# Kernel optimization log

Measured on AMD Instinct MI355X. Metric: run time of the kernel, lower is better.

Reference implementation:

```python
import jax, jax.numpy as jnp
import numpy as np

B, S, D, U = 64, 2048, 512, 512

def setup_inputs() -> dict:
    key = jax.random.key(0)
    ks = jax.random.split(key, 8)
    query = jax.random.normal(ks[0], (B, D), dtype=jnp.float32)
    values = jax.random.normal(ks[1], (B, S, D), dtype=jnp.float32)
    # Keras Dense params (glorot-like scale), with biases (Dense default use_bias=True)
    W1 = jax.random.normal(ks[2], (D, U), dtype=jnp.float32) / np.sqrt(D)
    b1 = jnp.zeros((U,), dtype=jnp.float32)
    W2 = jax.random.normal(ks[3], (D, U), dtype=jnp.float32) / np.sqrt(D)
    b2 = jnp.zeros((U,), dtype=jnp.float32)
    V = jax.random.normal(ks[4], (U, 1), dtype=jnp.float32) / np.sqrt(U)
    bv = jnp.zeros((1,), dtype=jnp.float32)
    return {"query": query, "values": values, "W1": W1, "b1": b1,
            "W2": W2, "b2": b2, "V": V, "bv": bv}

def reference(query, values, W1, b1, W2, b2, V, bv) -> jnp.ndarray:
    # query: [B, D], values: [B, S, D]
    q_proj = query @ W1 + b1                      # [B, U]
    v_proj = jnp.einsum('bsd,du->bsu', values, W2) + b2  # [B, S, U]
    h = jnp.tanh(q_proj[:, None, :] + v_proj)     # [B, S, U]
    scores = jnp.einsum('bsu,uo->bso', h, V) + bv # [B, S, 1]
    attn = jax.nn.softmax(scores, axis=1)         # softmax over sequence axis
    context = jnp.sum(attn * values, axis=1)      # [B, D]
    return context
```

## Files before the change

kernel.cpp:

```cpp
#include <hip/hip_runtime.h>
#include <hip/hip_bf16.h>

#define BB 64
#define SS 2048
#define DD 512
#define UU 512
#define BS (BB*SS)

typedef __attribute__((ext_vector_type(8))) short bf16x8;
typedef __attribute__((ext_vector_type(4))) float f32x4;

static __device__ __forceinline__ unsigned short f2bf(float x) {
    union { float f; unsigned int u; } v; v.f = x;
    unsigned int r = v.u + 0x7FFFu + ((v.u >> 16) & 1u);
    return (unsigned short)(r >> 16);
}

__global__ void k_prep(const float* __restrict__ W2, unsigned short* __restrict__ W2T,
                       const float* __restrict__ query, const float* __restrict__ W1,
                       const float* __restrict__ b1, const float* __restrict__ b2,
                       float* __restrict__ qpb) {
    __shared__ float tile[64][65];
    const int t = threadIdx.x;
    if (blockIdx.x < 64) {
        const int ti = blockIdx.x >> 3;
        const int tj = blockIdx.x & 7;
        #pragma unroll
        for (int i = 0; i < 16; ++i) {
            int e = i*256 + t;
            int dr = e >> 6, uc = e & 63;
            tile[dr][uc] = W2[(size_t)(ti*64+dr)*UU + tj*64+uc];
        }
        __syncthreads();
        #pragma unroll
        for (int i = 0; i < 16; ++i) {
            int e = i*256 + t;
            int ur = e >> 6, dc = e & 63;
            W2T[(size_t)(tj*64+ur)*DD + ti*64+dc] = f2bf(tile[dc][ur]);
        }
    } else {
        const int b = blockIdx.x - 64;
        float a0 = 0.f, a1 = 0.f;
        for (int d = 0; d < DD; ++d) {
            float q = query[b*DD + d];
            a0 += q * W1[(size_t)d*UU + t];
            a1 += q * W1[(size_t)d*UU + t + 256];
        }
        qpb[b*UU + t]       = a0 + b1[t]     + b2[t];
        qpb[b*UU + t + 256] = a1 + b1[t+256] + b2[t+256];
    }
}

__launch_bounds__(256, 2)
__global__ void k_scores(const float* __restrict__ values,
                         const unsigned short* __restrict__ W2T,
                         const float* __restrict__ qpb,
                         const float* __restrict__ Vw,
                         float* __restrict__ scores) {
    __shared__ unsigned short Albuf[64*512];
    const int t  = threadIdx.x;
    const int m0 = blockIdx.x * 64;
    const int b  = m0 >> 11;

    const int wave = t >> 6, lane = t & 63;
    const int ln15 = lane & 15, quad = lane >> 4;

    float qv[2][4], vw[2][4];
    #pragma unroll
    for (int nc = 0; nc < 2; ++nc)
        #pragma unroll
        for (int nt = 0; nt < 4; ++nt) {
            int n = nc*256 + wave*64 + nt*16 + ln15;
            qv[nc][nt] = qpb[b*UU + n];
            vw[nc][nt] = Vw[n];
        }

    const float* src = values + (size_t)m0 * DD;
    #pragma unroll
    for (int i = 0; i < 16; ++i) {
        int gf  = i*256 + t;
        int row = gf >> 6;
        int g   = gf & 63;
        const float4 f0 = *(const float4*)(src + (size_t)row*DD + g*8);
        const float4 f1 = *(const float4*)(src + (size_t)row*DD + g*8 + 4);
        ushort4 lo, hi;
        lo.x = f2bf(f0.x); lo.y = f2bf(f0.y); lo.z = f2bf(f0.z); lo.w = f2bf(f0.w);
        hi.x = f2bf(f1.x); hi.y = f2bf(f1.y); hi.z = f2bf(f1.z); hi.w = f2bf(f1.w);
        int gs = g ^ (row & 7);
        ushort4* dst = (ushort4*)&Albuf[row*512 + gs*8];
        dst[0] = lo; dst[1] = hi;
    }
    __syncthreads();

    const unsigned short* bp[4];
    #pragma unroll
    for (int nt = 0; nt < 4; ++nt)
        bp[nt] = W2T + (size_t)(wave*64 + nt*16 + ln15) * DD + quad*8;

    int abase[4];
    #pragma unroll
    for (int mt = 0; mt < 4; ++mt)
        abase[mt] = (mt*16 + ln15) * 512;
    const int xm = ln15 & 7;

    float sacc[4][4] = {};

    bf16x8 bb[2][4];
    #pragma unroll
    for (int nt = 0; nt < 4; ++nt)
        bb[0][nt] = *(const bf16x8*)(bp[nt]);

    for (int nc = 0; nc < 2; ++nc) {
        f32x4 acc[4][4];
        #pragma unroll
        for (int mt = 0; mt < 4; ++mt)
            #pragma unroll
            for (int nt = 0; nt < 4; ++nt)
                acc[mt][nt] = f32x4{0.f, 0.f, 0.f, 0.f};

        #pragma unroll
        for (int ks = 0; ks < 16; ++ks) {
            const int j   = nc*16 + ks;
            const int cur = j & 1;
            if (j + 1 < 32) {
                const int jn  = j + 1;
                const int off = (jn >> 4) * (256*DD) + (jn & 15) * 32;
                #pragma unroll
                for (int nt = 0; nt < 4; ++nt)
                    bb[cur ^ 1][nt] = *(const bf16x8*)(bp[nt] + off);
            }
            bf16x8 afr[4];
            const int g4 = ks*4 + quad;
            #pragma unroll
            for (int mt = 0; mt < 4; ++mt)
                afr[mt] = *(const bf16x8*)&Albuf[abase[mt] + ((g4 ^ xm) << 3)];
            #pragma unroll
            for (int mt = 0; mt < 4; ++mt)
                #pragma unroll
                for (int nt = 0; nt < 4; ++nt)
                    acc[mt][nt] = __builtin_amdgcn_mfma_f32_16x16x32_bf16(
                        afr[mt], bb[cur][nt], acc[mt][nt], 0, 0, 0);
        }

        #pragma unroll
        for (int nt = 0; nt < 4; ++nt) {
            const float q = qv[nc][nt];
            const float w = vw[nc][nt];
            #pragma unroll
            for (int mt = 0; mt < 4; ++mt)
                #pragma unroll
                for (int r = 0; r < 4; ++r) {
                    float x = q + acc[mt][nt][r];
                    float e = __expf(x + x);
                    float rc = __builtin_amdgcn_rcpf(e + 1.f);
                    sacc[mt][r] = fmaf(fmaf(-2.f, rc, 1.f), w, sacc[mt][r]);
                }
        }
    }

    __syncthreads();
    float* buf = (float*)Albuf;
    #pragma unroll
    for (int mt = 0; mt < 4; ++mt)
        #pragma unroll
        for (int r = 0; r < 4; ++r) {
            float v = sacc[mt][r];
            v += __shfl_xor(v, 1);
            v += __shfl_xor(v, 2);
            v += __shfl_xor(v, 4);
            v += __shfl_xor(v, 8);
            if (ln15 == 0) buf[wave*64 + mt*16 + quad*4 + r] = v;
        }
    __syncthreads();
    if (t < 64)
        scores[m0 + t] = buf[t] + buf[64 + t] + buf[128 + t] + buf[192 + t];
}

__launch_bounds__(256)
__global__ void k_context(const float* __restrict__ values, const float* __restrict__ scores,
                          float* __restrict__ out) {
    __shared__ float w[SS];
    __shared__ float red8[8];
    __shared__ float4 red[16][16];
    const int blk = blockIdx.x;
    const int b = blk >> 3, d0 = (blk & 7) * 64;
    const int t = threadIdx.x;

    const float* sc = scores + b*SS;
    float v[8];
    float mx = -1e30f;
    #pragma unroll
    for (int i = 0; i < 8; ++i) { v[i] = sc[i*256 + t]; mx = fmaxf(mx, v[i]); }
    #pragma unroll
    for (int off = 32; off; off >>= 1) mx = fmaxf(mx, __shfl_xor(mx, off));
    if ((t & 63) == 0) red8[t >> 6] = mx;
    __syncthreads();
    mx = fmaxf(fmaxf(red8[0], red8[1]), fmaxf(red8[2], red8[3]));
    float sum = 0.f;
    #pragma unroll
    for (int i = 0; i < 8; ++i) { v[i] = __expf(v[i] - mx); sum += v[i]; }
    #pragma unroll
    for (int off = 32; off; off >>= 1) sum += __shfl_xor(sum, off);
    __syncthreads();
    if ((t & 63) == 0) red8[4 + (t >> 6)] = sum;
    __syncthreads();
    sum = red8[4] + red8[5] + red8[6] + red8[7];
    float inv = 1.f / sum;
    #pragma unroll
    for (int i = 0; i < 8; ++i) w[i*256 + t] = v[i] * inv;
    __syncthreads();

    const int di = t & 15, sg = t >> 4;
    float4 acc = make_float4(0.f, 0.f, 0.f, 0.f);
    const float* vb = values + (size_t)b*SS*DD + d0 + di*4;
    #pragma unroll 8
    for (int s = sg; s < SS; s += 16) {
        float wgt = w[s];
        float4 vv = *(const float4*)(vb + (size_t)s*DD);
        acc.x += wgt*vv.x; acc.y += wgt*vv.y; acc.z += wgt*vv.z; acc.w += wgt*vv.w;
    }
    red[sg][di] = acc;
    __syncthreads();
    if (t < 16) {
        float4 s4 = make_float4(0.f, 0.f, 0.f, 0.f);
        #pragma unroll
        for (int g = 0; g < 16; ++g) {
            float4 vv = red[g][t];
            s4.x += vv.x; s4.y += vv.y; s4.z += vv.z; s4.w += vv.w;
        }
        *(float4*)(out + (size_t)b*DD + d0 + t*4) = s4;
    }
}

extern "C" void kernel_launch(void* const* d_in, const int* in_sizes, int n_in,
                              void* d_out, int out_size, void* d_ws, size_t ws_size,
                              hipStream_t stream) {
    const float* query  = (const float*)d_in[0];
    const float* values = (const float*)d_in[1];
    const float* W1     = (const float*)d_in[2];
    const float* b1     = (const float*)d_in[3];
    const float* W2     = (const float*)d_in[4];
    const float* b2     = (const float*)d_in[5];
    const float* Vw     = (const float*)d_in[6];

    char* ws = (char*)d_ws;
    unsigned short* W2T = (unsigned short*)ws;
    float* qpb    = (float*)(ws + 524288);
    float* scores = (float*)(ws + 524288 + 131072);
    float* out    = (float*)d_out;

    k_prep<<<128, 256, 0, stream>>>(W2, W2T, query, W1, b1, b2, qpb);
    k_scores<<<BS/64, 256, 0, stream>>>(values, W2T, qpb, Vw, scores);
    k_context<<<BB*8, 256, 0, stream>>>(values, scores, out);
}
```

Measured before the change: 585.0 us.

## Fuse context accumulation into scores kernel with split softmax and 32x32 MFMA

The scores kernel now computes a block-local softmax (max, sum) over its 64 rows and immediately accumulates the weighted sum of the values rows it already has cached, writing partial context vectors. A small finish kernel then combines the 32 partials per batch with a log-sum-exp rescale. This removes the second full pass over the values tensor from global memory. The GEMM also switches to 32x32x16 MFMA with W2 pre-swizzled into a fragment-ordered layout, so B fragments are loaded with contiguous per-lane reads. The cost is extra partial-buffer traffic and a slightly different order of floating-point summation.

```diff
diff --git a/kernel.cpp b/kernel.cpp
--- a/kernel.cpp
+++ b/kernel.cpp
@@ -8,7 +8,7 @@
 #define BS (BB*SS)
 
 typedef __attribute__((ext_vector_type(8))) short bf16x8;
-typedef __attribute__((ext_vector_type(4))) float f32x4;
+typedef __attribute__((ext_vector_type(16))) float f32x16;
 
 static __device__ __forceinline__ unsigned short f2bf(float x) {
     union { float f; unsigned int u; } v; v.f = x;
@@ -16,7 +16,7 @@
     return (unsigned short)(r >> 16);
 }
 
-__global__ void k_prep(const float* __restrict__ W2, unsigned short* __restrict__ W2T,
+__global__ void k_prep(const float* __restrict__ W2, unsigned short* __restrict__ W2F,
                        const float* __restrict__ query, const float* __restrict__ W1,
                        const float* __restrict__ b1, const float* __restrict__ b2,
                        float* __restrict__ qpb) {
@@ -32,11 +32,17 @@
             tile[dr][uc] = W2[(size_t)(ti*64+dr)*UU + tj*64+uc];
         }
         __syncthreads();
-        #pragma unroll
-        for (int i = 0; i < 16; ++i) {
-            int e = i*256 + t;
-            int ur = e >> 6, dc = e & 63;
-            W2T[(size_t)(tj*64+ur)*DD + ti*64+dc] = f2bf(tile[dc][ur]);
+        const int ksl = t >> 6, ln = t & 63;
+        const int lh = ln >> 5, l31 = ln & 31;
+        #pragma unroll
+        for (int ntl = 0; ntl < 2; ++ntl) {
+            const int ks = ti*4 + ksl;
+            const int ntile = tj*2 + ntl;
+            bf16x8 g;
+            #pragma unroll
+            for (int j = 0; j < 8; ++j)
+                g[j] = (short)f2bf(tile[ksl*16 + lh*8 + j][ntl*32 + l31]);
+            *(bf16x8*)&W2F[(size_t)(((ks*16 + ntile)*64 + ln) * 8)] = g;
         }
     } else {
         const int b = blockIdx.x - 64;
@@ -53,27 +59,35 @@
 
 __launch_bounds__(256, 2)
 __global__ void k_scores(const float* __restrict__ values,
-                         const unsigned short* __restrict__ W2T,
+                         const unsigned short* __restrict__ W2F,
                          const float* __restrict__ qpb,
                          const float* __restrict__ Vw,
-                         float* __restrict__ scores) {
+                         float* __restrict__ pm, float* __restrict__ pl,
+                         float* __restrict__ pv) {
     __shared__ unsigned short Albuf[64*512];
-    const int t  = threadIdx.x;
-    const int m0 = blockIdx.x * 64;
-    const int b  = m0 >> 11;
-
+    const int t   = threadIdx.x;
+    const int blk = blockIdx.x;
+    const int m0  = blk * 64;
+    const int b   = blk >> 5;
     const int wave = t >> 6, lane = t & 63;
-    const int ln15 = lane & 15, quad = lane >> 4;
-
-    float qv[2][4], vw[2][4];
-    #pragma unroll
-    for (int nc = 0; nc < 2; ++nc)
-        #pragma unroll
-        for (int nt = 0; nt < 4; ++nt) {
-            int n = nc*256 + wave*64 + nt*16 + ln15;
-            qv[nc][nt] = qpb[b*UU + n];
-            vw[nc][nt] = Vw[n];
-        }
+    const int ln31 = lane & 31, half = lane >> 5;
+
+    const bf16x8* Bp = (const bf16x8*)W2F;
+    bf16x8 bfr[2][4];
+    #pragma unroll
+    for (int nt = 0; nt < 4; ++nt)
+        bfr[0][nt] = Bp[(0*16 + wave*4 + nt)*64 + lane];
+    #pragma unroll
+    for (int nt = 0; nt < 4; ++nt)
+        bfr[1][nt] = Bp[(1*16 + wave*4 + nt)*64 + lane];
+
+    float qv[4], vw[4];
+    #pragma unroll
+    for (int nt = 0; nt < 4; ++nt) {
+        int n = wave*128 + nt*32 + ln31;
+        qv[nt] = qpb[b*UU + n];
+        vw[nt] = Vw[n];
+    }
 
     const float* src = values + (size_t)m0 * DD;
     #pragma unroll
@@ -83,153 +97,127 @@
         int g   = gf & 63;
         const float4 f0 = *(const float4*)(src + (size_t)row*DD + g*8);
         const float4 f1 = *(const float4*)(src + (size_t)row*DD + g*8 + 4);
-        ushort4 lo, hi;
-        lo.x = f2bf(f0.x); lo.y = f2bf(f0.y); lo.z = f2bf(f0.z); lo.w = f2bf(f0.w);
-        hi.x = f2bf(f1.x); hi.y = f2bf(f1.y); hi.z = f2bf(f1.z); hi.w = f2bf(f1.w);
-        int gs = g ^ (row & 7);
-        ushort4* dst = (ushort4*)&Albuf[row*512 + gs*8];
-        dst[0] = lo; dst[1] = hi;
-    }
-    __syncthreads();
-
-    const unsigned short* bp[4];
-    #pragma unroll
-    for (int nt = 0; nt < 4; ++nt)
-        bp[nt] = W2T + (size_t)(wave*64 + nt*16 + ln15) * DD + quad*8;
-
-    int abase[4];
-    #pragma unroll
-    for (int mt = 0; mt < 4; ++mt)
-        abase[mt] = (mt*16 + ln15) * 512;
-    const int xm = ln15 & 7;
-
-    float sacc[4][4] = {};
-
-    bf16x8 bb[2][4];
-    #pragma unroll
-    for (int nt = 0; nt < 4; ++nt)
-        bb[0][nt] = *(const bf16x8*)(bp[nt]);
-
-    for (int nc = 0; nc < 2; ++nc) {
-        f32x4 acc[4][4];
-        #pragma unroll
-        for (int mt = 0; mt < 4; ++mt)
+        bf16x8 pk;
+        pk[0] = (short)f2bf(f0.x); pk[1] = (short)f2bf(f0.y);
+        pk[2] = (short)f2bf(f0.z); pk[3] = (short)f2bf(f0.w);
+        pk[4] = (short)f2bf(f1.x); pk[5] = (short)f2bf(f1.y);
+        pk[6] = (short)f2bf(f1.z); pk[7] = (short)f2bf(f1.w);
+        *(bf16x8*)&Albuf[row*512 + ((g ^ (row & 7)) << 3)] = pk;
+    }
+    __syncthreads();
+
+    f32x16 acc[2][4];
+    #pragma unroll
+    for (int mt = 0; mt < 2; ++mt)
+        #pragma unroll
+        for (int nt = 0; nt < 4; ++nt)
             #pragma unroll
-            for (int nt = 0; nt < 4; ++nt)
-                acc[mt][nt] = f32x4{0.f, 0.f, 0.f, 0.f};
-
-        #pragma unroll
-        for (int ks = 0; ks < 16; ++ks) {
-            const int j   = nc*16 + ks;
-            const int cur = j & 1;
-            if (j + 1 < 32) {
-                const int jn  = j + 1;
-                const int off = (jn >> 4) * (256*DD) + (jn & 15) * 32;
-                #pragma unroll
-                for (int nt = 0; nt < 4; ++nt)
-                    bb[cur ^ 1][nt] = *(const bf16x8*)(bp[nt] + off);
+            for (int r = 0; r < 16; ++r)
+                acc[mt][nt][r] = 0.f;
+
+    const int xm = ln31 & 7;
+    #pragma unroll 4
+    for (int ks = 0; ks < 32; ++ks) {
+        const int cur = ks & 1;
+        const int g8 = (((ks*2 + half) ^ xm) << 3);
+        bf16x8 a0 = *(const bf16x8*)&Albuf[ln31*512 + g8];
+        bf16x8 a1 = *(const bf16x8*)&Albuf[16384 + ln31*512 + g8];
+        #pragma unroll
+        for (int nt = 0; nt < 4; ++nt) {
+            acc[0][nt] = __builtin_amdgcn_mfma_f32_32x32x16_bf16(a0, bfr[cur][nt], acc[0][nt], 0, 0, 0);
+            acc[1][nt] = __builtin_amdgcn_mfma_f32_32x32x16_bf16(a1, bfr[cur][nt], acc[1][nt], 0, 0, 0);
+        }
+        #pragma unroll
+        for (int nt = 0; nt < 4; ++nt)
+            bfr[cur][nt] = Bp[((ks+2)*16 + wave*4 + nt)*64 + lane];
+    }
+
+    float sacc[2][16];
+    #pragma unroll
+    for (int mt = 0; mt < 2; ++mt)
+        #pragma unroll
+        for (int r = 0; r < 16; ++r)
+            sacc[mt][r] = 0.f;
+    #pragma unroll
+    for (int nt = 0; nt < 4; ++nt) {
+        const float q = qv[nt], w = vw[nt];
+        #pragma unroll
+        for (int mt = 0; mt < 2; ++mt)
+            #pragma unroll
+            for (int r = 0; r < 16; ++r) {
+                float x = q + acc[mt][nt][r];
+                float e = __expf(x + x);
+                float rc = __builtin_amdgcn_rcpf(e + 1.f);
+                sacc[mt][r] = fmaf(fmaf(-2.f, rc, 1.f), w, sacc[mt][r]);
             }
-            bf16x8 afr[4];
-            const int g4 = ks*4 + quad;
-            #pragma unroll
-            for (int mt = 0; mt < 4; ++mt)
-                afr[mt] = *(const bf16x8*)&Albuf[abase[mt] + ((g4 ^ xm) << 3)];
-            #pragma unroll
-            for (int mt = 0; mt < 4; ++mt)
-                #pragma unroll
-                for (int nt = 0; nt < 4; ++nt)
-                    acc[mt][nt] = __builtin_amdgcn_mfma_f32_16x16x32_bf16(
-                        afr[mt], bb[cur][nt], acc[mt][nt], 0, 0, 0);
-        }
-
-        #pragma unroll
-        for (int nt = 0; nt < 4; ++nt) {
-            const float q = qv[nc][nt];
-            const float w = vw[nc][nt];
-            #pragma unroll
-            for (int mt = 0; mt < 4; ++mt)
-                #pragma unroll
-                for (int r = 0; r < 4; ++r) {
-                    float x = q + acc[mt][nt][r];
-                    float e = __expf(x + x);
-                    float rc = __builtin_amdgcn_rcpf(e + 1.f);
-                    sacc[mt][r] = fmaf(fmaf(-2.f, rc, 1.f), w, sacc[mt][r]);
-                }
-        }
-    }
-
-    __syncthreads();
-    float* buf = (float*)Albuf;
-    #pragma unroll
-    for (int mt = 0; mt < 4; ++mt)
-        #pragma unroll
-        for (int r = 0; r < 4; ++r) {
+    }
+
+    __syncthreads();
+    float* sred = (float*)Albuf;
+    #pragma unroll
+    for (int mt = 0; mt < 2; ++mt)
+        #pragma unroll
+        for (int r = 0; r < 16; ++r) {
             float v = sacc[mt][r];
             v += __shfl_xor(v, 1);
             v += __shfl_xor(v, 2);
             v += __shfl_xor(v, 4);
             v += __shfl_xor(v, 8);
-            if (ln15 == 0) buf[wave*64 + mt*16 + quad*4 + r] = v;
-        }
-    __syncthreads();
-    if (t < 64)
-        scores[m0 + t] = buf[t] + buf[64 + t] + buf[128 + t] + buf[192 + t];
-}
-
-__launch_bounds__(256)
-__global__ void k_context(const float* __restrict__ values, const float* __restrict__ scores,
-                          float* __restrict__ out) {
-    __shared__ float w[SS];
-    __shared__ float red8[8];
-    __shared__ float4 red[16][16];
-    const int blk = blockIdx.x;
-    const int b = blk >> 3, d0 = (blk & 7) * 64;
-    const int t = threadIdx.x;
-
-    const float* sc = scores + b*SS;
-    float v[8];
-    float mx = -1e30f;
-    #pragma unroll
-    for (int i = 0; i < 8; ++i) { v[i] = sc[i*256 + t]; mx = fmaxf(mx, v[i]); }
-    #pragma unroll
-    for (int off = 32; off; off >>= 1) mx = fmaxf(mx, __shfl_xor(mx, off));
-    if ((t & 63) == 0) red8[t >> 6] = mx;
-    __syncthreads();
-    mx = fmaxf(fmaxf(red8[0], red8[1]), fmaxf(red8[2], red8[3]));
-    float sum = 0.f;
-    #pragma unroll
-    for (int i = 0; i < 8; ++i) { v[i] = __expf(v[i] - mx); sum += v[i]; }
-    #pragma unroll
-    for (int off = 32; off; off >>= 1) sum += __shfl_xor(sum, off);
-    __syncthreads();
-    if ((t & 63) == 0) red8[4 + (t >> 6)] = sum;
-    __syncthreads();
-    sum = red8[4] + red8[5] + red8[6] + red8[7];
-    float inv = 1.f / sum;
-    #pragma unroll
-    for (int i = 0; i < 8; ++i) w[i*256 + t] = v[i] * inv;
-    __syncthreads();
-
-    const int di = t & 15, sg = t >> 4;
-    float4 acc = make_float4(0.f, 0.f, 0.f, 0.f);
-    const float* vb = values + (size_t)b*SS*DD + d0 + di*4;
+            v += __shfl_xor(v, 16);
+            if (ln31 == 0)
+                sred[wave*64 + mt*32 + (r & 3) + 8*(r >> 2) + 4*half] = v;
+        }
+    __syncthreads();
+
+    if (t < 64) {
+        float s = sred[t] + sred[64 + t] + sred[128 + t] + sred[192 + t];
+        float m = s;
+        #pragma unroll
+        for (int off = 32; off; off >>= 1) m = fmaxf(m, __shfl_xor(m, off));
+        float p = __expf(s - m);
+        float l = p;
+        #pragma unroll
+        for (int off = 32; off; off >>= 1) l += __shfl_xor(l, off);
+        sred[256 + t] = p;
+        if (t == 0) { pm[blk] = m; pl[blk] = l; }
+    }
+    __syncthreads();
+
+    float2 cacc = make_float2(0.f, 0.f);
+    const float* vrow = values + (size_t)m0*DD + t*2;
     #pragma unroll 8
-    for (int s = sg; s < SS; s += 16) {
-        float wgt = w[s];
-        float4 vv = *(const float4*)(vb + (size_t)s*DD);
-        acc.x += wgt*vv.x; acc.y += wgt*vv.y; acc.z += wgt*vv.z; acc.w += wgt*vv.w;
-    }
-    red[sg][di] = acc;
-    __syncthreads();
-    if (t < 16) {
-        float4 s4 = make_float4(0.f, 0.f, 0.f, 0.f);
-        #pragma unroll
-        for (int g = 0; g < 16; ++g) {
-            float4 vv = red[g][t];
-            s4.x += vv.x; s4.y += vv.y; s4.z += vv.z; s4.w += vv.w;
-        }
-        *(float4*)(out + (size_t)b*DD + d0 + t*4) = s4;
-    }
+    for (int i = 0; i < 64; ++i) {
+        float p = sred[256 + i];
+        float2 v = *(const float2*)(vrow + (size_t)i*DD);
+        cacc.x = fmaf(p, v.x, cacc.x);
+        cacc.y = fmaf(p, v.y, cacc.y);
+    }
+    *(float2*)&pv[(size_t)blk*DD + t*2] = cacc;
+}
+
+__global__ void k_finish(const float* __restrict__ pv, const float* __restrict__ pm,
+                         const float* __restrict__ pl, float* __restrict__ out) {
+    __shared__ float sm_[32], sl_[32], sw[32];
+    const int b = blockIdx.x, t = threadIdx.x;
+    if (t < 32) { sm_[t] = pm[b*32 + t]; sl_[t] = pl[b*32 + t]; }
+    __syncthreads();
+    float M = -1e30f;
+    #pragma unroll
+    for (int c = 0; c < 32; ++c) M = fmaxf(M, sm_[c]);
+    float L = 0.f;
+    #pragma unroll
+    for (int c = 0; c < 32; ++c) L += sl_[c] * __expf(sm_[c] - M);
+    if (t < 32) sw[t] = __expf(sm_[t] - M) / L;
+    __syncthreads();
+    float2 a = make_float2(0.f, 0.f);
+    #pragma unroll 4
+    for (int c = 0; c < 32; ++c) {
+        float w = sw[c];
+        float2 v = *(const float2*)&pv[(size_t)(b*32 + c)*DD + t*2];
+        a.x = fmaf(w, v.x, a.x);
+        a.y = fmaf(w, v.y, a.y);
+    }
+    *(float2*)&out[(size_t)b*DD + t*2] = a;
 }
 
 extern "C" void kernel_launch(void* const* d_in, const int* in_sizes, int n_in,
@@ -244,12 +232,13 @@
     const float* Vw     = (const float*)d_in[6];
 
     char* ws = (char*)d_ws;
-    unsigned short* W2T = (unsigned short*)ws;
-    float* qpb    = (float*)(ws + 524288);
-    float* scores = (float*)(ws + 524288 + 131072);
-    float* out    = (float*)d_out;
-
-    k_prep<<<128, 256, 0, stream>>>(W2, W2T, query, W1, b1, b2, qpb);
-    k_scores<<<BS/64, 256, 0, stream>>>(values, W2T, qpb, Vw, scores);
-    k_context<<<BB*8, 256, 0, stream>>>(values, scores, out);
-}
+    unsigned short* W2F = (unsigned short*)ws;
+    float* qpb = (float*)(ws + 557056);
+    float* pm  = (float*)(ws + 557056 + 131072);
+    float* pl  = (float*)(ws + 557056 + 131072 + 8192);
+    float* pv  = (float*)(ws + 557056 + 131072 + 16384);
+
+    k_prep<<<128, 256, 0, stream>>>(W2, W2F, query, W1, b1, b2, qpb);
+    k_scores<<<BS/64, 256, 0, stream>>>(values, W2F, qpb, Vw, pm, pl, pv);
+    k_finish<<<BB, 256, 0, stream>>>(pv, pm, pl, (float*)d_out);
+}
```

Result: faster. 510.1 us (-12.8%).
